# Kernel optimization log

Measured on AMD Instinct MI355X. Metric: run time of the kernel, lower is better.

## Reference

```python
import jax, jax.numpy as jnp
import numpy as np

B = 32      # graphs per batch
N_NODES = 1024  # nodes per graph
K = 16      # top-k edges per node


def setup_inputs() -> dict:
    key = jax.random.key(0)
    k1, k2 = jax.random.split(key)
    x = jax.random.normal(k1, (B * N_NODES, 128), dtype=jnp.float32) * 0.1
    W = jax.random.normal(k2, (128, 64), dtype=jnp.float32) * (1.0 / np.sqrt(128))
    b = jnp.zeros((64,), dtype=jnp.float32)
    temperature = jnp.asarray(4.0, dtype=jnp.float32)
    return {"x": x, "W": W, "b": b, "temperature": temperature}


def reference(x, W, b, temperature):
    # Encoder: linear node embedding. out: [B*n, C]
    out = x @ W + b
    C = out.shape[-1]
    # Per-graph features, detached as in the original (graph_x = out[...].detach())
    h = jax.lax.stop_gradient(out).reshape(B, N_NODES, C)
    # Pairwise squared euclidean distances per graph: d[b,i,j] = ||h_i - h_j||^2
    sq = jnp.sum(h * h, axis=-1)  # [B, n]
    d_e = sq[:, :, None] + sq[:, None, :] - 2.0 * jnp.einsum('bic,bjc->bij', h, h)
    logits = jnp.exp(-temperature * d_e)  # [B, n, n]
    # Gumbel-noised top-k edge sampling
    z = jax.random.gumbel(jax.random.key(1), logits.shape, logits.dtype)
    _, edges_hat = jax.lax.top_k(logits + z, K)  # [B, n, K] int32
    # Build global edge index with cumulative per-graph node offsets
    offsets = (jnp.arange(B, dtype=jnp.int32) * N_NODES)[:, None, None]  # [B,1,1]
    rows = jnp.broadcast_to(jnp.arange(N_NODES, dtype=jnp.int32)[None, :, None] + offsets,
                            (B, N_NODES, K))
    cols = edges_hat.astype(jnp.int32) + offsets
    edges_idx = jnp.stack((rows.reshape(-1), cols.reshape(-1)))  # [2, B*n*K]
    return out, edges_idx
```

## Files before the change

kernel.cpp:

```cpp
#include <hip/hip_runtime.h>
#include <math.h>

#define OUT_ELEMS 2097152
#define EDGE_ELEMS 524288

__device__ __forceinline__ unsigned int rotl32(unsigned int x, int r){
  return (x << r) | (x >> (32 - r));
}

__device__ __forceinline__ unsigned int tf_bits_part(unsigned int e){
  unsigned int x0 = 0u, x1 = e;
  const unsigned int ks1 = 1u;
  const unsigned int ks2 = 0x1BD11BDBu;
  x1 += ks1;
#define TFR(r) { x0 += x1; x1 = rotl32(x1, r); x1 ^= x0; }
  TFR(13) TFR(15) TFR(26) TFR(6)
  x0 += ks1; x1 += ks2 + 1u;
  TFR(17) TFR(29) TFR(16) TFR(24)
  x0 += ks2; x1 += 0u + 2u;
  TFR(13) TFR(15) TFR(26) TFR(6)
  x0 += 0u;  x1 += ks1 + 3u;
  TFR(17) TFR(29) TFR(16) TFR(24)
  x0 += ks1; x1 += ks2 + 4u;
  TFR(13) TFR(15) TFR(26) TFR(6)
  x0 += ks2; x1 += 0u + 5u;
#undef TFR
  return x0 ^ x1;
}

__device__ __forceinline__ double rcp64(double x){
  double r;
  asm("v_rcp_f64 %0, %1" : "=v"(r) : "v"(x));
  double e = fma(-x, r, 1.0); r = fma(r, e, r);
  e = fma(-x, r, 1.0); r = fma(r, e, r);
  return r;
}

__device__ __forceinline__ double fast_exp(double x){
  double fn = __builtin_rint(x * 1.4426950408889634);
  int n = (int)fn;
  double r = fma(fn, -0.6931471803691238, x);
  r = fma(fn, -1.9082149292705877e-10, r);
  double p = 2.7557319223985893e-06;
  p = fma(r, p, 2.4801587301587302e-05);
  p = fma(r, p, 1.9841269841269841e-04);
  p = fma(r, p, 1.3888888888888889e-03);
  p = fma(r, p, 8.3333333333333333e-03);
  p = fma(r, p, 4.1666666666666664e-02);
  p = fma(r, p, 1.6666666666666666e-01);
  p = fma(r, p, 0.5);
  p = fma(r, p, 1.0);
  p = fma(r, p, 1.0);
  double scale = __longlong_as_double(((long long)(n + 1023)) << 52);
  return p * scale;
}

__device__ __forceinline__ double fast_log(double x){
  long long bx = __double_as_longlong(x);
  long long e = (bx >> 52) - 1023;
  double m = __longlong_as_double((bx & 0xFFFFFFFFFFFFFll) |
                                  0x3FF0000000000000ll);
  int big = m > 1.4142135623730951;
  m = big ? 0.5 * m : m;
  e += big;
  double s = (m - 1.0) * rcp64(m + 1.0);
  double s2 = s * s;
  double p = fma(s2, 2.0/11.0, 2.0/9.0);
  p = fma(s2, p, 2.0/7.0);
  p = fma(s2, p, 2.0/5.0);
  p = fma(s2, p, 2.0/3.0);
  double lm = fma(s * s2, p, 2.0 * s);
  return fma((double)e, 0.6931471805599453, lm);
}

__device__ __forceinline__ float dist2_f32(
    const float* __restrict__ og, const float* __restrict__ hrowf,
    unsigned int jc){
  const float4* cp4 = (const float4*)(og + ((size_t)jc << 6));
  const float4* hp4 = (const float4*)hrowf;
  float a0 = 0.0f, a1 = 0.0f, a2 = 0.0f, a3 = 0.0f;
  #pragma unroll 4
  for (int ch = 0; ch < 16; ++ch){
    float4 cf = cp4[ch];
    float4 hf = hp4[ch];
    float d0 = hf.x - cf.x;
    float d1 = hf.y - cf.y;
    float d2 = hf.z - cf.z;
    float d3 = hf.w - cf.w;
    a0 = fmaf(d0, d0, a0);
    a1 = fmaf(d1, d1, a1);
    a2 = fmaf(d2, d2, a2);
    a3 = fmaf(d3, d3, a3);
  }
  return (a0 + a1) + (a2 + a3);
}

__device__ __forceinline__ unsigned long long pack_key(double sc,
                                                       unsigned int jc){
  unsigned long long kb = (unsigned long long)__double_as_longlong(sc);
  kb ^= (unsigned long long)(((long long)kb) >> 63) | 0x8000000000000000ull;
  return (kb & ~1023ull) | (unsigned long long)(1023u - jc);
}

__device__ __forceinline__ unsigned long long tail64(
    float accf, unsigned int bits, unsigned int jc, double Td, bool act){
  if (!act) return 0ull;
  double sgm = fast_exp(-Td * (double)accf);
  float f = __uint_as_float(0x3f800000u | (bits >> 9)) - 1.0f;
  double u = (f > 0.0f) ? (double)f : 1.1754943508222875e-38;
  double w = -fast_log(u);
  double z = -fast_log(w);
  double sc = sgm + z;
  return pack_key(sc, jc);
}

__device__ __forceinline__ unsigned long long tail32(
    float accf, unsigned int bits, unsigned int jc, float Tf, bool act){
  if (!act) return 0ull;
  float sg = __expf(-Tf * accf);
  float f = __uint_as_float(0x3f800000u | (bits >> 9)) - 1.0f;
  float uf = (f > 0.0f) ? f : 1.17549435e-38f;
  float wv = -__logf(uf);
  float zf = -__logf(wv);
  double sc = (double)sg + (double)zf;
  return pack_key(sc, jc);
}

__device__ __forceinline__ double key_score(unsigned long long k){
  unsigned long long orig = (k >> 63) ? (k ^ 0x8000000000000000ull) : ~k;
  return __longlong_as_double((long long)(orig & ~1023ull));
}

__device__ __forceinline__ unsigned long long bitonic64_desc(
    unsigned long long key, int lane){
  #pragma unroll
  for (int k = 2; k <= 64; k <<= 1){
    #pragma unroll
    for (int j = k >> 1; j; j >>= 1){
      unsigned long long o = __shfl_xor(key, j, 64);
      bool keep_hi = ((lane & k) == 0) == ((lane & j) == 0);
      key = (keep_hi == (o > key)) ? o : key;
    }
  }
  return key;
}

__device__ __forceinline__ unsigned int bitonic32_desc(
    unsigned int key, int lane){
  #pragma unroll
  for (int k = 2; k <= 64; k <<= 1){
    #pragma unroll
    for (int j = k >> 1; j; j >>= 1){
      unsigned int o = __shfl_xor(key, j, 64);
      bool keep_hi = ((lane & k) == 0) == ((lane & j) == 0);
      key = (keep_hi == (o > key)) ? o : key;
    }
  }
  return key;
}

__global__ __launch_bounds__(256) void cvt_wb_v19(
    const float* __restrict__ W, const float* __restrict__ b,
    double* __restrict__ w64, double* __restrict__ b64){
  const int i = blockIdx.x * 256 + threadIdx.x;
  if (i < 8192)      w64[i] = (double)W[i];
  else if (i < 8256) b64[i - 8192] = (double)b[i - 8192];
}

__global__ __launch_bounds__(512, 8) void encoder_v19(
    const float* __restrict__ x, const double* __restrict__ w64,
    const double* __restrict__ b64, float* __restrict__ out){
  __shared__ float xs[64 * 129];
  const int tid = threadIdx.x;
  const int rblk = blockIdx.x >> 1;
  const int cblk = (blockIdx.x & 1) << 5;

  {
    const float4* xg4 = (const float4*)(x + ((size_t)rblk << 13));
    #pragma unroll
    for (int s = 0; s < 4; ++s){
      const int idx = tid + (s << 9);
      float4 v = xg4[idx];
      const int r = idx >> 5, k4 = (idx & 31) << 2;
      float* p = &xs[r * 129 + k4];
      p[0] = v.x; p[1] = v.y; p[2] = v.z; p[3] = v.w;
    }
  }
  __syncthreads();

  const int lane = tid & 63;
  const int wu = __builtin_amdgcn_readfirstlane(tid >> 6);
  const int c0 = cblk + (wu << 2);
  const size_t row = ((size_t)rblk << 6) + (size_t)lane;

  double acc[4];
  const double* __restrict__ bp = b64 + c0;
  #pragma unroll
  for (int j = 0; j < 4; ++j) acc[j] = bp[j];

  const float* __restrict__ xrow = &xs[lane * 129];
  #pragma unroll 4
  for (int k = 0; k < 128; ++k){
    const double xk = (double)xrow[k];
    const double* __restrict__ wp = w64 + (k << 6) + c0;
    #pragma unroll
    for (int j = 0; j < 4; ++j)
      acc[j] = fma(xk, wp[j], acc[j]);
  }

  float* __restrict__ orow = out + (row << 6) + c0;
  float4 st;
  st.x = (float)acc[0]; st.y = (float)acc[1];
  st.z = (float)acc[2]; st.w = (float)acc[3];
  *(float4*)orow = st;
}

__global__ __launch_bounds__(256, 8) void edges_v19(
    const float* __restrict__ out32, const float* __restrict__ temp,
    float* __restrict__ rows_out, float* __restrict__ cols_out){
  __shared__ float hidf[4][64];
  __shared__ unsigned int cl[4][128];
  const int tid = threadIdx.x, wave = tid >> 6, lane = tid & 63;
  const int gb = blockIdx.x >> 8;
  const int i0 = (blockIdx.x & 255) << 2;
  const int r  = i0 + wave;
  const float* __restrict__ og = out32 + ((size_t)gb << 16);

  hidf[wave][lane] = og[((size_t)r << 6) + lane];

  const unsigned int base = ((unsigned int)gb << 20) | ((unsigned int)r << 10);

  unsigned int v[16];
  unsigned int pmax = 0u;
  #pragma unroll
  for (int m = 0; m < 16; ++m){
    const unsigned int j = (unsigned int)(m << 6) + (unsigned int)lane;
    unsigned int bits = tf_bits_part(base | j);
    v[m] = (bits & ~1023u) | (1023u - j);
    pmax = (v[m] > pmax) ? v[m] : pmax;
  }

  unsigned int sorted = bitonic32_desc(pmax, lane);
  unsigned int b16p = __shfl(sorted, 15, 64);

  float u16 = __uint_as_float(0x3f800000u | (b16p >> 9)) - 1.0f;
  float z16 = -__logf(-__logf(u16));
  float uc  = __expf(-__expf(-(z16 - 1.001f)));
  unsigned int cp = ((__float_as_uint(1.0f + uc) & 0x7FFFFFu) << 9) & ~1023u;

  int cnt = 0;
  #pragma unroll
  for (int m = 0; m < 16; ++m) cnt += (v[m] >= cp) ? 1 : 0;
  int s = cnt;
  #pragma unroll
  for (int off = 1; off < 64; off <<= 1){
    int o = __shfl_up(s, off, 64);
    s += (lane >= off) ? o : 0;
  }
  int nc = __shfl(s, 63, 64);
  nc = (nc > 128) ? 128 : nc;
  int slot = s - cnt;
  #pragma unroll
  for (int m = 0; m < 16; ++m){
    if (v[m] >= cp && slot < 128){
      cl[wave][slot] = 1023u - (v[m] & 1023u);
      ++slot;
    }
  }

  const double Td = (double)temp[0];
  const float  Tf = temp[0];
  unsigned long long key;

  if (nc <= 64){
    const bool act1 = (lane < nc);
    const unsigned int jc1 = act1 ? cl[wave][lane] : 0u;
    const float ac1 = dist2_f32(og, &hidf[wave][0], jc1);
    const unsigned int bt1 = tf_bits_part(base | jc1);
    key = tail32(ac1, bt1, jc1, Tf, act1);
    key = bitonic64_desc(key, lane);
    double s0 = key_score(key);
    unsigned long long kn = __shfl_down(key, 1, 64);
    double s1 = key_score(kn);
    bool tight = (lane < 16) && (key != 0ull) && ((s0 - s1) < 4e-5);
    if (__any(tight)){
      key = tail64(ac1, bt1, jc1, Td, act1);
      key = bitonic64_desc(key, lane);
    }
  } else {
    const bool act1 = (lane < nc);
    const unsigned int jc1 = act1 ? cl[wave][lane] : 0u;
    const float ac1 = dist2_f32(og, &hidf[wave][0], jc1);
    const unsigned int bt1 = tf_bits_part(base | jc1);
    key = tail64(ac1, bt1, jc1, Td, act1);
    key = bitonic64_desc(key, lane);

    const int idx2 = 64 + lane;
    const bool act2 = (idx2 < nc);
    const unsigned int jc2 = act2 ? cl[wave][idx2] : 0u;
    const float ac2 = dist2_f32(og, &hidf[wave][0], jc2);
    const unsigned int bt2 = tf_bits_part(base | jc2);
    unsigned long long k2 = tail64(ac2, bt2, jc2, Td, act2);
    k2 = bitonic64_desc(k2, lane);
    unsigned long long kr = __shfl(k2, 63 - lane, 64);
    key = (kr > key) ? kr : key;
    #pragma unroll
    for (int j2 = 32; j2; j2 >>= 1){
      unsigned long long o = __shfl_xor(key, j2, 64);
      bool left = (lane & j2) == 0;
      bool take = left ? (o > key) : (o < key);
      key = take ? o : key;
    }
  }

  const int grow = (gb << 10) + r;
  if (lane < 16){
    rows_out[((size_t)grow << 4) + lane] = (float)grow;
    cols_out[((size_t)grow << 4) + lane] =
        (float)((gb << 10) + (1023 - (int)(key & 1023ull)));
  }
}

extern "C" void kernel_launch(void* const* d_in, const int* in_sizes, int n_in,
                              void* d_out, int out_size, void* d_ws, size_t ws_size,
                              hipStream_t stream){
  const float* x = (const float*)d_in[0];
  const float* W = (const float*)d_in[1];
  const float* b = (const float*)d_in[2];
  const float* T = (const float*)d_in[3];
  float* out      = (float*)d_out;
  float* rows_out = out + OUT_ELEMS;
  float* cols_out = rows_out + EDGE_ELEMS;

  double* w64 = (double*)d_ws;
  double* b64 = w64 + 8192;

  cvt_wb_v19<<<33, 256, 0, stream>>>(W, b, w64, b64);
  encoder_v19<<<1024, 512, 0, stream>>>(x, w64, b64, out);
  edges_v19<<<8192, 256, 0, stream>>>(out, T, rows_out, cols_out);
}
```

Before: 179.0 us.

## Fuse weight conversion into encoder and stage fp64 weight slice in LDS

Removes the separate kernel that converted W and b to double in workspace. The encoder now converts a 128x16 column slice of W to double directly into shared memory. Each thread reads its own x row from global memory as float4 instead of staging x tiles in LDS. This drops one launch and the workspace round-trip. The cost is that every block converts W redundantly, and the per-thread x reads are strided across lanes, so they are uncoalesced.

```diff
diff --git a/kernel.cpp b/kernel.cpp
--- a/kernel.cpp
+++ b/kernel.cpp
@@ -159,63 +159,66 @@
   return key;
 }
 
-__global__ __launch_bounds__(256) void cvt_wb_v19(
-    const float* __restrict__ W, const float* __restrict__ b,
-    double* __restrict__ w64, double* __restrict__ b64){
-  const int i = blockIdx.x * 256 + threadIdx.x;
-  if (i < 8192)      w64[i] = (double)W[i];
-  else if (i < 8256) b64[i - 8192] = (double)b[i - 8192];
-}
-
-__global__ __launch_bounds__(512, 8) void encoder_v19(
-    const float* __restrict__ x, const double* __restrict__ w64,
-    const double* __restrict__ b64, float* __restrict__ out){
-  __shared__ float xs[64 * 129];
+__global__ __launch_bounds__(256, 6) void encoder_v20(
+    const float* __restrict__ x, const float* __restrict__ W,
+    const float* __restrict__ b, float* __restrict__ out){
+  __shared__ double Wl[128 * 16];
   const int tid = threadIdx.x;
-  const int rblk = blockIdx.x >> 1;
-  const int cblk = (blockIdx.x & 1) << 5;
+  const int rt = blockIdx.x >> 2;
+  const int cb = (blockIdx.x & 3) << 4;
 
   {
-    const float4* xg4 = (const float4*)(x + ((size_t)rblk << 13));
-    #pragma unroll
-    for (int s = 0; s < 4; ++s){
-      const int idx = tid + (s << 9);
-      float4 v = xg4[idx];
-      const int r = idx >> 5, k4 = (idx & 31) << 2;
-      float* p = &xs[r * 129 + k4];
-      p[0] = v.x; p[1] = v.y; p[2] = v.z; p[3] = v.w;
+    #pragma unroll
+    for (int s = 0; s < 8; ++s){
+      const int idx = tid + (s << 8);
+      const int k = idx >> 4, c = idx & 15;
+      Wl[idx] = (double)W[(k << 6) + cb + c];
     }
   }
   __syncthreads();
 
   const int lane = tid & 63;
-  const int wu = __builtin_amdgcn_readfirstlane(tid >> 6);
-  const int c0 = cblk + (wu << 2);
-  const size_t row = ((size_t)rblk << 6) + (size_t)lane;
+  const int wv = tid >> 6;
+  const int wc = wv << 2;
+  const size_t row = ((size_t)rt << 6) + (size_t)lane;
+  const float4* __restrict__ xg = (const float4*)(x + (row << 7));
 
   double acc[4];
-  const double* __restrict__ bp = b64 + c0;
-  #pragma unroll
-  for (int j = 0; j < 4; ++j) acc[j] = bp[j];
-
-  const float* __restrict__ xrow = &xs[lane * 129];
-  #pragma unroll 4
-  for (int k = 0; k < 128; ++k){
-    const double xk = (double)xrow[k];
-    const double* __restrict__ wp = w64 + (k << 6) + c0;
-    #pragma unroll
-    for (int j = 0; j < 4; ++j)
-      acc[j] = fma(xk, wp[j], acc[j]);
-  }
-
-  float* __restrict__ orow = out + (row << 6) + c0;
+  #pragma unroll
+  for (int j = 0; j < 4; ++j) acc[j] = (double)b[cb + wc + j];
+
+#define ENC_STEP(xf, krow) {                                   \
+    const double xk = (double)(xf);                            \
+    const double* __restrict__ wp = &Wl[((krow) << 4) + wc];   \
+    acc[0] = fma(xk, wp[0], acc[0]);                           \
+    acc[1] = fma(xk, wp[1], acc[1]);                           \
+    acc[2] = fma(xk, wp[2], acc[2]);                           \
+    acc[3] = fma(xk, wp[3], acc[3]); }
+
+  #pragma unroll 2
+  for (int ch = 0; ch < 8; ++ch){
+    float4 xq[4];
+    #pragma unroll
+    for (int q = 0; q < 4; ++q) xq[q] = xg[(ch << 2) + q];
+    #pragma unroll
+    for (int q = 0; q < 4; ++q){
+      const int k0 = (ch << 4) + (q << 2);
+      ENC_STEP(xq[q].x, k0 + 0)
+      ENC_STEP(xq[q].y, k0 + 1)
+      ENC_STEP(xq[q].z, k0 + 2)
+      ENC_STEP(xq[q].w, k0 + 3)
+    }
+  }
+#undef ENC_STEP
+
+  float* __restrict__ orow = out + (row << 6) + cb + wc;
   float4 st;
   st.x = (float)acc[0]; st.y = (float)acc[1];
   st.z = (float)acc[2]; st.w = (float)acc[3];
   *(float4*)orow = st;
 }
 
-__global__ __launch_bounds__(256, 8) void edges_v19(
+__global__ __launch_bounds__(256, 8) void edges_v20(
     const float* __restrict__ out32, const float* __restrict__ temp,
     float* __restrict__ rows_out, float* __restrict__ cols_out){
   __shared__ float hidf[4][64];
@@ -332,10 +335,6 @@
   float* rows_out = out + OUT_ELEMS;
   float* cols_out = rows_out + EDGE_ELEMS;
 
-  double* w64 = (double*)d_ws;
-  double* b64 = w64 + 8192;
-
-  cvt_wb_v19<<<33, 256, 0, stream>>>(W, b, w64, b64);
-  encoder_v19<<<1024, 512, 0, stream>>>(x, w64, b64, out);
-  edges_v19<<<8192, 256, 0, stream>>>(out, T, rows_out, cols_out);
-}
+  encoder_v20<<<2048, 256, 0, stream>>>(x, W, b, out);
+  edges_v20<<<8192, 256, 0, stream>>>(out, T, rows_out, cols_out);
+}
```

Result: slower. 202.3 us (+13.0%).
